# Optimization experiments

Measured on AMD Instinct MI355X. Metric: run time of the kernel, lower is better.

Reference implementation:

```python
import jax, jax.numpy as jnp
import numpy as np

M = 8192       # nodes per graph
W_IN = 64      # input feature width (data.w)
HID = 32       # cfgs[i]
B = 16         # batch size
NNZ = 131072   # sparse Laplacian nonzeros (avg degree 16)
EXTRA = 32     # extra_input_size
EPS = 1e-5     # BatchNorm1d eps


def setup_inputs() -> dict:
    key = jax.random.key(0)
    ks = jax.random.split(key, 20)
    inp = {}
    inp["inputs"] = jax.random.normal(ks[0], (B, M, W_IN), jnp.float32)
    inp["ex_inputs"] = jax.random.normal(ks[1], (B, EXTRA), jnp.float32)
    inp["edge_row"] = jax.random.randint(ks[2], (NNZ,), 0, M, jnp.int32)
    inp["edge_col"] = jax.random.randint(ks[3], (NNZ,), 0, M, jnp.int32)
    inp["edge_val"] = jax.random.normal(ks[4], (NNZ,), jnp.float32) * 0.05
    # layer 0: Linear(W_IN -> HID) + BN(HID)
    inp["W1"] = jax.random.normal(ks[5], (W_IN, HID), jnp.float32) * 0.05
    inp["b1"] = jnp.zeros((HID,), jnp.float32)
    inp["g1"] = jnp.ones((HID,), jnp.float32)
    inp["be1"] = jnp.zeros((HID,), jnp.float32)
    # layer 1: Linear(HID -> HID) + BN(HID)
    inp["W2"] = jax.random.normal(ks[6], (HID, HID), jnp.float32) * 0.05
    inp["b2"] = jnp.zeros((HID,), jnp.float32)
    inp["g2"] = jnp.ones((HID,), jnp.float32)
    inp["be2"] = jnp.zeros((HID,), jnp.float32)
    # head
    inp["fc1_w"] = jax.random.normal(ks[7], (HID * M + EXTRA, 512), jnp.float32) * 0.01
    inp["fc1_b"] = jnp.zeros((512,), jnp.float32)
    inp["fc2_w"] = jax.random.normal(ks[8], (512, 2), jnp.float32) * 0.05
    inp["fc2_b"] = jnp.zeros((2,), jnp.float32)
    return inp


def _gcn_layer(x, edge_row, edge_col, edge_val, Wl, bl, g, be):
    # x: (B, m, f). Matches linear_layer + BN(train stats) + relu in torch code.
    bsz, m, f = x.shape
    xr = jnp.transpose(x, (1, 0, 2)).reshape(m, bsz * f)              # (m, B*f)
    Lx = jax.ops.segment_sum(edge_val[:, None] * xr[edge_col],
                             edge_row, num_segments=m)                # spmm (m, B*f)
    Lx = Lx.reshape(m * bsz, f) @ Wl + bl                             # Linear
    x = jnp.transpose(Lx.reshape(m, bsz, -1), (1, 0, 2))              # (B, m, HID)
    # BatchNorm1d over channel dim, stats over (batch, nodes) — training mode, biased var
    mean = x.mean(axis=(0, 1))
    var = ((x - mean) ** 2).mean(axis=(0, 1))
    x = g * (x - mean) * jax.lax.rsqrt(var + EPS) + be
    return jax.nn.relu(x)


def reference(inputs, ex_inputs, edge_row, edge_col, edge_val,
              W1, b1, g1, be1, W2, b2, g2, be2,
              fc1_w, fc1_b, fc2_w, fc2_b):
    x = _gcn_layer(inputs, edge_row, edge_col, edge_val, W1, b1, g1, be1)
    x = _gcn_layer(x, edge_row, edge_col, edge_val, W2, b2, g2, be2)
    x = x.reshape(x.shape[0], -1)                                     # (B, m*HID)
    h = jax.nn.relu(jnp.concatenate([x, ex_inputs], axis=1) @ fc1_w + fc1_b)
    # dropout is identity (eval / p=0)
    return h @ fc2_w + fc2_b                                          # (B, 2)
```

## Files before the change

kernel.cpp:

```cpp
#include <hip/hip_runtime.h>

#define MM 8192
#define BATCH 16
#define HIDN 32
#define WIN 64
#define NNZ 131072
#define EXTRA 32
#define EPS 1e-5f
#define NSTAT 131072.0f

__global__ void k_zero(float* p, int n) {
    int i = blockIdx.x * 256 + threadIdx.x;
    if (i < n) p[i] = 0.f;
}

__global__ void k_hist(const int* __restrict__ row, int* cnt) {
    int e = blockIdx.x * 256 + threadIdx.x;
    atomicAdd(&cnt[row[e]], 1);
}

__global__ void k_scan(const int* __restrict__ cnt, int* __restrict__ ptr, int* __restrict__ cursor) {
    __shared__ int part[1024];
    int t = threadIdx.x;
    int base = t * 8;
    int pre[8];
    int s = 0;
#pragma unroll
    for (int i = 0; i < 8; i++) { pre[i] = s; s += cnt[base + i]; }
    part[t] = s;
    __syncthreads();
    for (int off = 1; off < 1024; off <<= 1) {
        int v = (t >= off) ? part[t - off] : 0;
        __syncthreads();
        part[t] += v;
        __syncthreads();
    }
    int offs = (t == 0) ? 0 : part[t - 1];
#pragma unroll
    for (int i = 0; i < 8; i++) {
        ptr[base + i] = offs + pre[i];
        cursor[base + i] = offs + pre[i];
    }
    if (t == 1023) ptr[8192] = part[1023];
}

__global__ void k_scatter(const int* __restrict__ row, const int* __restrict__ col,
                          const float* __restrict__ val, int* cursor,
                          int* __restrict__ csr_col, float* __restrict__ csr_val) {
    int e = blockIdx.x * 256 + threadIdx.x;
    int r = row[e];
    int p = atomicAdd(&cursor[r], 1);
    csr_col[p] = col[e];
    csr_val[p] = val[e];
}

__global__ __launch_bounds__(256) void k_lin1(const float* __restrict__ x,
                                              const float* __restrict__ W1,
                                              float* __restrict__ z) {
    __shared__ float xs[32 * 64];
    int t = threadIdx.x;
    int p0 = blockIdx.x * 32;
    const float4* x4 = (const float4*)(x + (size_t)p0 * 64);
    float4* xs4 = (float4*)xs;
    xs4[t] = x4[t];
    xs4[t + 256] = x4[t + 256];
    int lane = t & 63;
    int h = lane & 31;
    int sub = lane >> 5;
    int wv = t >> 6;
    float wcol[64];
#pragma unroll
    for (int f = 0; f < 64; f++) wcol[f] = W1[f * 32 + h];
    __syncthreads();
    int b = p0 >> 13;
    int m0 = p0 & 8191;
#pragma unroll
    for (int it = 0; it < 4; it++) {
        int pl = wv * 8 + it * 2 + sub;
        const float4* xr = (const float4*)(xs + pl * 64);
        float acc = 0.f;
#pragma unroll
        for (int i = 0; i < 16; i++) {
            float4 v = xr[i];
            acc += v.x * wcol[4*i] + v.y * wcol[4*i+1] + v.z * wcol[4*i+2] + v.w * wcol[4*i+3];
        }
        z[(size_t)(m0 + pl) * 512 + b * 32 + h] = acc;
    }
}

__global__ __launch_bounds__(256) void k_spmm(const float* __restrict__ z,
                                              const int* __restrict__ ptr,
                                              const int* __restrict__ cols,
                                              const float* __restrict__ vals,
                                              float* __restrict__ y) {
    int t = threadIdx.x;
    int lane = t & 63;
    int r = blockIdx.x * 4 + (t >> 6);
    int e0 = ptr[r], e1 = ptr[r + 1];
    float4 a0 = {0.f, 0.f, 0.f, 0.f};
    float4 a1 = {0.f, 0.f, 0.f, 0.f};
    const float4* z4 = (const float4*)z;
    for (int e = e0; e < e1; e++) {
        int c = cols[e];
        float v = vals[e];
        float4 b0 = z4[(size_t)c * 128 + lane];
        float4 b1 = z4[(size_t)c * 128 + 64 + lane];
        a0.x += v * b0.x; a0.y += v * b0.y; a0.z += v * b0.z; a0.w += v * b0.w;
        a1.x += v * b1.x; a1.y += v * b1.y; a1.z += v * b1.z; a1.w += v * b1.w;
    }
    float4* y4 = (float4*)y;
    y4[(size_t)r * 128 + lane] = a0;
    y4[(size_t)r * 128 + 64 + lane] = a1;
}

__global__ __launch_bounds__(256) void k_stats(const float* __restrict__ y, float* __restrict__ st) {
    int t = threadIdx.x;
    int idx = blockIdx.x * 256 + t;
    float s1 = 0.f, s2 = 0.f;
    for (int i = idx; i < MM * 512; i += 512 * 256) {
        float v = y[i];
        s1 += v; s2 += v * v;
    }
    s1 += __shfl_xor(s1, 32, 64);
    s2 += __shfl_xor(s2, 32, 64);
    __shared__ float ls[64];
    if (t < 64) ls[t] = 0.f;
    __syncthreads();
    int ch = t & 31;
    if ((t & 32) == 0) { atomicAdd(&ls[ch], s1); atomicAdd(&ls[32 + ch], s2); }
    __syncthreads();
    if (t < 64) atomicAdd(&st[t], ls[t]);
}

__global__ __launch_bounds__(256) void k_lin2(const float* __restrict__ y,
                                              const float* __restrict__ st,
                                              const float* __restrict__ g,
                                              const float* __restrict__ be,
                                              const float* __restrict__ W2,
                                              float* __restrict__ z) {
    __shared__ float xs[64 * 32];
    int t = threadIdx.x;
    int ch = t & 31;
    float mean = st[ch] * (1.f / NSTAT);
    float var = st[32 + ch] * (1.f / NSTAT) - mean * mean;
    float a = g[ch] * rsqrtf(var + EPS);
    float c = be[ch] - mean * a;
    int q0 = blockIdx.x * 64;
    const float* src = y + (size_t)q0 * 32;
#pragma unroll
    for (int i = 0; i < 8; i++) {
        float v = src[t + i * 256];
        xs[t + i * 256] = fmaxf(a * v + c, 0.f);
    }
    int lane = t & 63;
    int h2 = lane & 31;
    int sub = lane >> 5;
    int wv = t >> 6;
    float wcol[32];
#pragma unroll
    for (int h = 0; h < 32; h++) wcol[h] = W2[h * 32 + h2];
    __syncthreads();
    float* zo = z + (size_t)q0 * 32;
#pragma unroll
    for (int it = 0; it < 8; it++) {
        int ql = wv * 16 + it * 2 + sub;
        const float4* xr = (const float4*)(xs + ql * 32);
        float acc = 0.f;
#pragma unroll
        for (int i = 0; i < 8; i++) {
            float4 v = xr[i];
            acc += v.x * wcol[4*i] + v.y * wcol[4*i+1] + v.z * wcol[4*i+2] + v.w * wcol[4*i+3];
        }
        zo[ql * 32 + h2] = acc;
    }
}

__global__ __launch_bounds__(256) void k_head(const float* __restrict__ y,
                                              const float* __restrict__ st,
                                              const float* __restrict__ g,
                                              const float* __restrict__ be,
                                              const float* __restrict__ fw,
                                              float* __restrict__ partial) {
    __shared__ float xsh[16 * 512];
    int t = threadIdx.x;
    int ch = t & 31;
    float mean = st[ch] * (1.f / NSTAT);
    float var = st[32 + ch] * (1.f / NSTAT) - mean * mean;
    float a = g[ch] * rsqrtf(var + EPS);
    float c = be[ch] - mean * a;
    int m0 = blockIdx.x * 16;
#pragma unroll
    for (int mi = 0; mi < 16; mi++) {
        int m = m0 + mi;
        float v0 = y[(size_t)m * 512 + t];
        float v1 = y[(size_t)m * 512 + t + 256];
        xsh[mi * 512 + ch * 16 + (t >> 5)]     = fmaxf(a * v0 + c, 0.f);
        xsh[mi * 512 + ch * 16 + (t >> 5) + 8] = fmaxf(a * v1 + c, 0.f);
    }
    __syncthreads();
    int tcol = t & 127;
    int half = t >> 7;
    float4 acc[16];
#pragma unroll
    for (int b = 0; b < 16; b++) acc[b] = make_float4(0.f, 0.f, 0.f, 0.f);
    const float4* fw4 = (const float4*)fw;
    for (int mi = half * 8; mi < half * 8 + 8; mi++) {
        int m = m0 + mi;
        const float* xrow = xsh + mi * 512;
#pragma unroll 4
        for (int h = 0; h < 32; h++) {
            float4 w = fw4[(size_t)(m * 32 + h) * 128 + tcol];
            const float4* lt4 = (const float4*)(xrow + h * 16);
#pragma unroll
            for (int i = 0; i < 4; i++) {
                float4 Xi = lt4[i];
                acc[4*i+0].x += Xi.x * w.x; acc[4*i+0].y += Xi.x * w.y; acc[4*i+0].z += Xi.x * w.z; acc[4*i+0].w += Xi.x * w.w;
                acc[4*i+1].x += Xi.y * w.x; acc[4*i+1].y += Xi.y * w.y; acc[4*i+1].z += Xi.y * w.z; acc[4*i+1].w += Xi.y * w.w;
                acc[4*i+2].x += Xi.z * w.x; acc[4*i+2].y += Xi.z * w.y; acc[4*i+2].z += Xi.z * w.z; acc[4*i+2].w += Xi.z * w.w;
                acc[4*i+3].x += Xi.w * w.x; acc[4*i+3].y += Xi.w * w.y; acc[4*i+3].z += Xi.w * w.z; acc[4*i+3].w += Xi.w * w.w;
            }
        }
    }
    __syncthreads();
    float4* mrg = (float4*)xsh;
    if (half == 1) {
#pragma unroll
        for (int b = 0; b < 16; b++) mrg[b * 128 + tcol] = acc[b];
    }
    __syncthreads();
    if (half == 0) {
        float4* po = (float4*)(partial + (size_t)blockIdx.x * 8192);
#pragma unroll
        for (int b = 0; b < 16; b++) {
            float4 o = mrg[b * 128 + tcol];
            acc[b].x += o.x; acc[b].y += o.y; acc[b].z += o.z; acc[b].w += o.w;
            po[b * 128 + tcol] = acc[b];
        }
    }
}

__global__ __launch_bounds__(256) void k_red(const float* __restrict__ partial, float* __restrict__ red) {
    int tid = blockIdx.x * 256 + threadIdx.x;
    int elem = tid & 8191;
    int p8 = tid >> 13;
    const float* pp = partial + (size_t)p8 * 64 * 8192 + elem;
    float s0 = 0.f, s1 = 0.f, s2 = 0.f, s3 = 0.f;
    for (int k = 0; k < 64; k += 4) {
        s0 += pp[(size_t)(k + 0) * 8192];
        s1 += pp[(size_t)(k + 1) * 8192];
        s2 += pp[(size_t)(k + 2) * 8192];
        s3 += pp[(size_t)(k + 3) * 8192];
    }
    red[p8 * 8192 + elem] = (s0 + s1) + (s2 + s3);
}

__global__ __launch_bounds__(512) void k_final(const float* __restrict__ red,
                                               const float* __restrict__ ex,
                                               const float* __restrict__ fw,
                                               const float* __restrict__ fb1,
                                               const float* __restrict__ fw2,
                                               const float* __restrict__ fb2,
                                               float* __restrict__ out) {
    int b = blockIdx.x;
    int n = threadIdx.x;
    float v = fb1[n];
#pragma unroll
    for (int p = 0; p < 8; p++) v += red[p * 8192 + b * 512 + n];
#pragma unroll
    for (int e = 0; e < 32; e++)
        v += ex[b * 32 + e] * fw[(size_t)(262144 + e) * 512 + n];
    float h = fmaxf(v, 0.f);
    float p0 = h * fw2[n * 2];
    float p1 = h * fw2[n * 2 + 1];
#pragma unroll
    for (int off = 32; off > 0; off >>= 1) {
        p0 += __shfl_xor(p0, off, 64);
        p1 += __shfl_xor(p1, off, 64);
    }
    __shared__ float ls[16];
    int wv = n >> 6;
    if ((n & 63) == 0) { ls[wv * 2] = p0; ls[wv * 2 + 1] = p1; }
    __syncthreads();
    if (n == 0) {
        float s0 = 0.f, s1 = 0.f;
        for (int w = 0; w < 8; w++) { s0 += ls[w * 2]; s1 += ls[w * 2 + 1]; }
        out[b * 2 + 0] = s0 + fb2[0];
        out[b * 2 + 1] = s1 + fb2[1];
    }
}

extern "C" void kernel_launch(void* const* d_in, const int* in_sizes, int n_in,
                              void* d_out, int out_size, void* d_ws, size_t ws_size,
                              hipStream_t stream) {
    const float* inputs = (const float*)d_in[0];
    const float* ex     = (const float*)d_in[1];
    const int*   erow   = (const int*)d_in[2];
    const int*   ecol   = (const int*)d_in[3];
    const float* evalp  = (const float*)d_in[4];
    const float* W1     = (const float*)d_in[5];
    const float* g1     = (const float*)d_in[7];
    const float* be1    = (const float*)d_in[8];
    const float* W2     = (const float*)d_in[9];
    const float* g2     = (const float*)d_in[11];
    const float* be2    = (const float*)d_in[12];
    const float* fc1w   = (const float*)d_in[13];
    const float* fc1b   = (const float*)d_in[14];
    const float* fc2w   = (const float*)d_in[15];
    const float* fc2b   = (const float*)d_in[16];
    float* out = (float*)d_out;

    float* zbuf    = (float*)d_ws;
    float* ybuf    = zbuf + (size_t)MM * 512;
    int*   row_cnt = (int*)(ybuf + (size_t)MM * 512);
    float* stats   = (float*)(row_cnt + 8192);
    int*   row_ptr = (int*)(stats + 128);
    int*   cursor  = row_ptr + 8193;
    int*   csr_col = cursor + 8192;
    float* csr_val = (float*)(csr_col + NNZ);
    float* red     = csr_val + NNZ;

    k_zero<<<(8320 + 255) / 256, 256, 0, stream>>>((float*)row_cnt, 8320);
    k_hist<<<NNZ / 256, 256, 0, stream>>>(erow, row_cnt);
    k_scan<<<1, 1024, 0, stream>>>(row_cnt, row_ptr, cursor);
    k_scatter<<<NNZ / 256, 256, 0, stream>>>(erow, ecol, evalp, cursor, csr_col, csr_val);
    k_lin1<<<4096, 256, 0, stream>>>(inputs, W1, zbuf);
    k_spmm<<<2048, 256, 0, stream>>>(zbuf, row_ptr, csr_col, csr_val, ybuf);
    k_stats<<<512, 256, 0, stream>>>(ybuf, stats);
    k_lin2<<<2048, 256, 0, stream>>>(ybuf, stats, g1, be1, W2, zbuf);
    k_spmm<<<2048, 256, 0, stream>>>(zbuf, row_ptr, csr_col, csr_val, ybuf);
    k_stats<<<512, 256, 0, stream>>>(ybuf, stats + 64);
    k_head<<<512, 256, 0, stream>>>(ybuf, stats + 64, g2, be2, fc1w, zbuf);
    k_red<<<256, 256, 0, stream>>>(zbuf, red);
    k_final<<<16, 512, 0, stream>>>(red, ex, fc1w, fc1b, fc2w, fc2b, out);
}
```

Baseline: 908.3 us.

## Fuse BatchNorm statistics into SpMM and batch-load CSR indices via shuffles

```diff
diff --git a/kernel.cpp b/kernel.cpp
--- a/kernel.cpp
+++ b/kernel.cpp
@@ -92,44 +92,64 @@
                                               const int* __restrict__ ptr,
                                               const int* __restrict__ cols,
                                               const float* __restrict__ vals,
-                                              float* __restrict__ y) {
-    int t = threadIdx.x;
+                                              float* __restrict__ y,
+                                              float* __restrict__ st) {
+    __shared__ float ls[64];
+    int t = threadIdx.x;
+    if (t < 64) ls[t] = 0.f;
     int lane = t & 63;
     int r = blockIdx.x * 4 + (t >> 6);
     int e0 = ptr[r], e1 = ptr[r + 1];
     float4 a0 = {0.f, 0.f, 0.f, 0.f};
     float4 a1 = {0.f, 0.f, 0.f, 0.f};
     const float4* z4 = (const float4*)z;
-    for (int e = e0; e < e1; e++) {
-        int c = cols[e];
-        float v = vals[e];
-        float4 b0 = z4[(size_t)c * 128 + lane];
-        float4 b1 = z4[(size_t)c * 128 + 64 + lane];
-        a0.x += v * b0.x; a0.y += v * b0.y; a0.z += v * b0.z; a0.w += v * b0.w;
-        a1.x += v * b1.x; a1.y += v * b1.y; a1.z += v * b1.z; a1.w += v * b1.w;
+    for (int base = e0; base < e1; base += 64) {
+        int n = e1 - base; if (n > 64) n = 64;
+        int myc = 0; float myv = 0.f;
+        if (lane < n) { myc = cols[base + lane]; myv = vals[base + lane]; }
+        for (int j = 0; j < n; j++) {
+            int c = __shfl(myc, j, 64);
+            float v = __shfl(myv, j, 64);
+            float4 b0 = z4[(size_t)c * 128 + lane];
+            float4 b1 = z4[(size_t)c * 128 + 64 + lane];
+            a0.x += v * b0.x; a0.y += v * b0.y; a0.z += v * b0.z; a0.w += v * b0.w;
+            a1.x += v * b1.x; a1.y += v * b1.y; a1.z += v * b1.z; a1.w += v * b1.w;
+        }
     }
     float4* y4 = (float4*)y;
     y4[(size_t)r * 128 + lane] = a0;
     y4[(size_t)r * 128 + 64 + lane] = a1;
-}
-
-__global__ __launch_bounds__(256) void k_stats(const float* __restrict__ y, float* __restrict__ st) {
-    int t = threadIdx.x;
-    int idx = blockIdx.x * 256 + t;
+    float4 s = {a0.x + a1.x, a0.y + a1.y, a0.z + a1.z, a0.w + a1.w};
+    float4 q = {a0.x*a0.x + a1.x*a1.x, a0.y*a0.y + a1.y*a1.y,
+                a0.z*a0.z + a1.z*a1.z, a0.w*a0.w + a1.w*a1.w};
+#pragma unroll
+    for (int off = 8; off <= 32; off <<= 1) {
+        s.x += __shfl_xor(s.x, off, 64); s.y += __shfl_xor(s.y, off, 64);
+        s.z += __shfl_xor(s.z, off, 64); s.w += __shfl_xor(s.w, off, 64);
+        q.x += __shfl_xor(q.x, off, 64); q.y += __shfl_xor(q.y, off, 64);
+        q.z += __shfl_xor(q.z, off, 64); q.w += __shfl_xor(q.w, off, 64);
+    }
+    __syncthreads();
+    if (lane < 8) {
+        int ch = lane * 4;
+        atomicAdd(&ls[ch + 0], s.x); atomicAdd(&ls[ch + 1], s.y);
+        atomicAdd(&ls[ch + 2], s.z); atomicAdd(&ls[ch + 3], s.w);
+        atomicAdd(&ls[32 + ch + 0], q.x); atomicAdd(&ls[32 + ch + 1], q.y);
+        atomicAdd(&ls[32 + ch + 2], q.z); atomicAdd(&ls[32 + ch + 3], q.w);
+    }
+    __syncthreads();
+    if (t < 64) atomicAdd(&st[(blockIdx.x & 7) * 64 + t], ls[t]);
+}
+
+__device__ inline void bn_coef(const float* st, const float* g, const float* be,
+                               int ch, float& a, float& c) {
     float s1 = 0.f, s2 = 0.f;
-    for (int i = idx; i < MM * 512; i += 512 * 256) {
-        float v = y[i];
-        s1 += v; s2 += v * v;
-    }
-    s1 += __shfl_xor(s1, 32, 64);
-    s2 += __shfl_xor(s2, 32, 64);
-    __shared__ float ls[64];
-    if (t < 64) ls[t] = 0.f;
-    __syncthreads();
-    int ch = t & 31;
-    if ((t & 32) == 0) { atomicAdd(&ls[ch], s1); atomicAdd(&ls[32 + ch], s2); }
-    __syncthreads();
-    if (t < 64) atomicAdd(&st[t], ls[t]);
+#pragma unroll
+    for (int cp = 0; cp < 8; cp++) { s1 += st[cp * 64 + ch]; s2 += st[cp * 64 + 32 + ch]; }
+    float mean = s1 * (1.f / NSTAT);
+    float var = s2 * (1.f / NSTAT) - mean * mean;
+    a = g[ch] * rsqrtf(var + EPS);
+    c = be[ch] - mean * a;
 }
 
 __global__ __launch_bounds__(256) void k_lin2(const float* __restrict__ y,
@@ -141,10 +161,8 @@
     __shared__ float xs[64 * 32];
     int t = threadIdx.x;
     int ch = t & 31;
-    float mean = st[ch] * (1.f / NSTAT);
-    float var = st[32 + ch] * (1.f / NSTAT) - mean * mean;
-    float a = g[ch] * rsqrtf(var + EPS);
-    float c = be[ch] - mean * a;
+    float a, c;
+    bn_coef(st, g, be, ch, a, c);
     int q0 = blockIdx.x * 64;
     const float* src = y + (size_t)q0 * 32;
 #pragma unroll
@@ -184,10 +202,8 @@
     __shared__ float xsh[16 * 512];
     int t = threadIdx.x;
     int ch = t & 31;
-    float mean = st[ch] * (1.f / NSTAT);
-    float var = st[32 + ch] * (1.f / NSTAT) - mean * mean;
-    float a = g[ch] * rsqrtf(var + EPS);
-    float c = be[ch] - mean * a;
+    float a, c;
+    bn_coef(st, g, be, ch, a, c);
     int m0 = blockIdx.x * 16;
 #pragma unroll
     for (int mi = 0; mi < 16; mi++) {
@@ -313,23 +329,21 @@
     float* ybuf    = zbuf + (size_t)MM * 512;
     int*   row_cnt = (int*)(ybuf + (size_t)MM * 512);
     float* stats   = (float*)(row_cnt + 8192);
-    int*   row_ptr = (int*)(stats + 128);
+    int*   row_ptr = (int*)(stats + 1024);
     int*   cursor  = row_ptr + 8193;
     int*   csr_col = cursor + 8192;
     float* csr_val = (float*)(csr_col + NNZ);
     float* red     = csr_val + NNZ;
 
-    k_zero<<<(8320 + 255) / 256, 256, 0, stream>>>((float*)row_cnt, 8320);
+    k_zero<<<(9216 + 255) / 256, 256, 0, stream>>>((float*)row_cnt, 9216);
     k_hist<<<NNZ / 256, 256, 0, stream>>>(erow, row_cnt);
     k_scan<<<1, 1024, 0, stream>>>(row_cnt, row_ptr, cursor);
     k_scatter<<<NNZ / 256, 256, 0, stream>>>(erow, ecol, evalp, cursor, csr_col, csr_val);
     k_lin1<<<4096, 256, 0, stream>>>(inputs, W1, zbuf);
-    k_spmm<<<2048, 256, 0, stream>>>(zbuf, row_ptr, csr_col, csr_val, ybuf);
-    k_stats<<<512, 256, 0, stream>>>(ybuf, stats);
+    k_spmm<<<2048, 256, 0, stream>>>(zbuf, row_ptr, csr_col, csr_val, ybuf, stats);
     k_lin2<<<2048, 256, 0, stream>>>(ybuf, stats, g1, be1, W2, zbuf);
-    k_spmm<<<2048, 256, 0, stream>>>(zbuf, row_ptr, csr_col, csr_val, ybuf);
-    k_stats<<<512, 256, 0, stream>>>(ybuf, stats + 64);
-    k_head<<<512, 256, 0, stream>>>(ybuf, stats + 64, g2, be2, fc1w, zbuf);
+    k_spmm<<<2048, 256, 0, stream>>>(zbuf, row_ptr, csr_col, csr_val, ybuf, stats + 512);
+    k_head<<<512, 256, 0, stream>>>(ybuf, stats + 512, g2, be2, fc1w, zbuf);
     k_red<<<256, 256, 0, stream>>>(zbuf, red);
     k_final<<<16, 512, 0, stream>>>(red, ex, fc1w, fc1b, fc2w, fc2b, out);
 }
```

Measured after the change: 878.6 us. 3.3% less time.
